# Kernel tuning notes

Hardware: AMD Instinct MI355X
Metric: run time of the kernel (lower is better)

The kernel has to match this reference:

```python
import jax, jax.numpy as jnp
import numpy as np

N, C, H, W = 64, 64, 128, 128
KH, KW = 3, 3


def setup_inputs() -> dict:
    key = jax.random.key(0)
    k1, k2 = jax.random.split(key)
    images = jax.random.normal(k1, (N, C, H, W), dtype=jnp.float32)
    kernels = jax.random.normal(k2, (N, C, KH, KW), dtype=jnp.float32)
    return {"images": images, "kernels": kernels}


def reference(images, kernels):
    # Per-sample conv: image i ([C,H,W]) convolved with kernel i ([C,kh,kw]) -> 1 channel.
    # Equivalent to a grouped conv with N groups:
    #   input  [1, N*C, H, W], weights [N, C, kh, kw], feature_group_count=N
    n, c, h, w = images.shape
    x = images.reshape(1, n * c, h, w)
    out = jax.lax.conv_general_dilated(
        x, kernels,
        window_strides=(1, 1),
        padding='VALID',
        dimension_numbers=('NCHW', 'OIHW', 'NCHW'),
        feature_group_count=n,
    )  # [1, N, H', W']
    return out.reshape(n, 1, out.shape[2], out.shape[3])
```

## Files before the change

kernel.cpp:

```cpp
#include <hip/hip_runtime.h>


#define NS   64
#define CCH  64
#define HH   128
#define WW   128
#define OHH  126
#define OWW  126
#define CHS  (HH * WW)

__global__ __launch_bounds__(512, 4)
void ImageWiseConv2d_direct(const float* __restrict__ img,
                            const float* __restrict__ ker,
                            float* __restrict__ out)
{
    const int tid = threadIdx.x;
    const int bx  = blockIdx.x;
    const int bt  = bx & 7;
    const int n   = bx >> 3;
    const int h0  = bt * 16;

    const int r0 = tid >> 5;
    const int c0 = (tid & 31) << 2;

    int ihr = h0 + r0;
    if (ihr > HH - 3) ihr = HH - 3;
    const int bOff = (c0 < 124) ? 4 : 2;

    const float* p0 = img + (((n * CCH) * HH) + ihr) * WW + c0;
    const float* kp = ker + (n * CCH) * 9;

    float a0 = 0.f, a1 = 0.f, a2 = 0.f, a3 = 0.f;

    float4 A0, A1, A2;
    float2 B0, B1, B2;
    A0 = *(const float4*)(p0);
    A1 = *(const float4*)(p0 + WW);
    A2 = *(const float4*)(p0 + 2 * WW);
    B0 = *(const float2*)(p0 + bOff);
    B1 = *(const float2*)(p0 + WW + bOff);
    B2 = *(const float2*)(p0 + 2 * WW + bOff);

    for (int c = 0; c < CCH; ++c) {
        float4 nA0, nA1, nA2;
        float2 nB0, nB1, nB2;
        const bool more = (c + 1 < CCH);
        if (more) {
            const float* q = p0 + (c + 1) * CHS;
            nA0 = *(const float4*)(q);
            nA1 = *(const float4*)(q + WW);
            nA2 = *(const float4*)(q + 2 * WW);
            nB0 = *(const float2*)(q + bOff);
            nB1 = *(const float2*)(q + WW + bOff);
            nB2 = *(const float2*)(q + 2 * WW + bOff);
        }

        const float w0 = kp[c * 9 + 0], w1 = kp[c * 9 + 1], w2 = kp[c * 9 + 2];
        const float w3 = kp[c * 9 + 3], w4 = kp[c * 9 + 4], w5 = kp[c * 9 + 5];
        const float w6 = kp[c * 9 + 6], w7 = kp[c * 9 + 7], w8 = kp[c * 9 + 8];

        {
            const float v0 = A0.x, v1 = A0.y, v2 = A0.z, v3 = A0.w, v4 = B0.x, v5 = B0.y;
            a0 = fmaf(w0, v0, a0); a0 = fmaf(w1, v1, a0); a0 = fmaf(w2, v2, a0);
            a1 = fmaf(w0, v1, a1); a1 = fmaf(w1, v2, a1); a1 = fmaf(w2, v3, a1);
            a2 = fmaf(w0, v2, a2); a2 = fmaf(w1, v3, a2); a2 = fmaf(w2, v4, a2);
            a3 = fmaf(w0, v3, a3); a3 = fmaf(w1, v4, a3); a3 = fmaf(w2, v5, a3);
        }
        {
            const float v0 = A1.x, v1 = A1.y, v2 = A1.z, v3 = A1.w, v4 = B1.x, v5 = B1.y;
            a0 = fmaf(w3, v0, a0); a0 = fmaf(w4, v1, a0); a0 = fmaf(w5, v2, a0);
            a1 = fmaf(w3, v1, a1); a1 = fmaf(w4, v2, a1); a1 = fmaf(w5, v3, a1);
            a2 = fmaf(w3, v2, a2); a2 = fmaf(w4, v3, a2); a2 = fmaf(w5, v4, a2);
            a3 = fmaf(w3, v3, a3); a3 = fmaf(w4, v4, a3); a3 = fmaf(w5, v5, a3);
        }
        {
            const float v0 = A2.x, v1 = A2.y, v2 = A2.z, v3 = A2.w, v4 = B2.x, v5 = B2.y;
            a0 = fmaf(w6, v0, a0); a0 = fmaf(w7, v1, a0); a0 = fmaf(w8, v2, a0);
            a1 = fmaf(w6, v1, a1); a1 = fmaf(w7, v2, a1); a1 = fmaf(w8, v3, a1);
            a2 = fmaf(w6, v2, a2); a2 = fmaf(w7, v3, a2); a2 = fmaf(w8, v4, a2);
            a3 = fmaf(w6, v3, a3); a3 = fmaf(w7, v4, a3); a3 = fmaf(w8, v5, a3);
        }

        if (more) {
            A0 = nA0; A1 = nA1; A2 = nA2;
            B0 = nB0; B1 = nB1; B2 = nB2;
        }
    }

    const int oh = h0 + r0;
    if (oh < OHH) {
        float* o0 = out + (n * OHH + oh) * OWW + c0;
        *(float2*)o0 = make_float2(a0, a1);
        if (c0 < 124) {
            *(float2*)(o0 + 2) = make_float2(a2, a3);
        }
    }
}

extern "C" void kernel_launch(void* const* d_in, const int* in_sizes, int n_in,
                              void* d_out, int out_size, void* d_ws, size_t ws_size,
                              hipStream_t stream) {
    const float* img = (const float*)d_in[0];
    const float* ker = (const float*)d_in[1];
    float* out = (float*)d_out;

    ImageWiseConv2d_direct<<<dim3(NS * 8), dim3(512), 0, stream>>>(img, ker, out);
}
```

Measured before the change: 392.9 us.

## Compute two output rows per thread and fetch halo via lane shuffles

Each thread now computes a 2x4 output tile instead of 1x4. It loads 4 input rows per channel instead of 3 for each single output row, so the overlapping middle rows are reused from registers across both outputs. The float2 halo loads are replaced by __shfl_down from the neighbouring lane, which removes half the global load instructions. Blocks shrink to 256 threads to keep 16 rows per block. This halves total thread count and raises register pressure, which may reduce latency hiding for the streaming loads.

Result: faster. 354.9 us (median of 2 runs) (-9.7%).

```diff
diff --git a/kernel.cpp b/kernel.cpp
--- a/kernel.cpp
+++ b/kernel.cpp
@@ -9,7 +9,7 @@
 #define OWW  126
 #define CHS  (HH * WW)
 
-__global__ __launch_bounds__(512, 4)
+__global__ __launch_bounds__(256, 2)
 void ImageWiseConv2d_direct(const float* __restrict__ img,
                             const float* __restrict__ ker,
                             float* __restrict__ out)
@@ -20,79 +20,95 @@
     const int n   = bx >> 3;
     const int h0  = bt * 16;
 
-    const int r0 = tid >> 5;
+    const int r0 = (tid >> 5) << 1;
     const int c0 = (tid & 31) << 2;
 
     int ihr = h0 + r0;
-    if (ihr > HH - 3) ihr = HH - 3;
-    const int bOff = (c0 < 124) ? 4 : 2;
+    if (ihr > HH - 4) ihr = HH - 4;
 
     const float* p0 = img + (((n * CCH) * HH) + ihr) * WW + c0;
     const float* kp = ker + (n * CCH) * 9;
 
-    float a0 = 0.f, a1 = 0.f, a2 = 0.f, a3 = 0.f;
+    float a00 = 0.f, a01 = 0.f, a02 = 0.f, a03 = 0.f;
+    float a10 = 0.f, a11 = 0.f, a12 = 0.f, a13 = 0.f;
 
-    float4 A0, A1, A2;
-    float2 B0, B1, B2;
+    float4 A0, A1, A2, A3;
     A0 = *(const float4*)(p0);
     A1 = *(const float4*)(p0 + WW);
     A2 = *(const float4*)(p0 + 2 * WW);
-    B0 = *(const float2*)(p0 + bOff);
-    B1 = *(const float2*)(p0 + WW + bOff);
-    B2 = *(const float2*)(p0 + 2 * WW + bOff);
+    A3 = *(const float4*)(p0 + 3 * WW);
 
     for (int c = 0; c < CCH; ++c) {
-        float4 nA0, nA1, nA2;
-        float2 nB0, nB1, nB2;
+        float4 nA0, nA1, nA2, nA3;
         const bool more = (c + 1 < CCH);
         if (more) {
             const float* q = p0 + (c + 1) * CHS;
             nA0 = *(const float4*)(q);
             nA1 = *(const float4*)(q + WW);
             nA2 = *(const float4*)(q + 2 * WW);
-            nB0 = *(const float2*)(q + bOff);
-            nB1 = *(const float2*)(q + WW + bOff);
-            nB2 = *(const float2*)(q + 2 * WW + bOff);
+            nA3 = *(const float4*)(q + 3 * WW);
         }
 
         const float w0 = kp[c * 9 + 0], w1 = kp[c * 9 + 1], w2 = kp[c * 9 + 2];
         const float w3 = kp[c * 9 + 3], w4 = kp[c * 9 + 4], w5 = kp[c * 9 + 5];
         const float w6 = kp[c * 9 + 6], w7 = kp[c * 9 + 7], w8 = kp[c * 9 + 8];
 
+        const float h40 = __shfl_down(A0.x, 1), h50 = __shfl_down(A0.y, 1);
+        const float h41 = __shfl_down(A1.x, 1), h51 = __shfl_down(A1.y, 1);
+        const float h42 = __shfl_down(A2.x, 1), h52 = __shfl_down(A2.y, 1);
+        const float h43 = __shfl_down(A3.x, 1), h53 = __shfl_down(A3.y, 1);
+
         {
-            const float v0 = A0.x, v1 = A0.y, v2 = A0.z, v3 = A0.w, v4 = B0.x, v5 = B0.y;
-            a0 = fmaf(w0, v0, a0); a0 = fmaf(w1, v1, a0); a0 = fmaf(w2, v2, a0);
-            a1 = fmaf(w0, v1, a1); a1 = fmaf(w1, v2, a1); a1 = fmaf(w2, v3, a1);
-            a2 = fmaf(w0, v2, a2); a2 = fmaf(w1, v3, a2); a2 = fmaf(w2, v4, a2);
-            a3 = fmaf(w0, v3, a3); a3 = fmaf(w1, v4, a3); a3 = fmaf(w2, v5, a3);
+            const float v0 = A0.x, v1 = A0.y, v2 = A0.z, v3 = A0.w, v4 = h40, v5 = h50;
+            a00 = fmaf(w0, v0, a00); a00 = fmaf(w1, v1, a00); a00 = fmaf(w2, v2, a00);
+            a01 = fmaf(w0, v1, a01); a01 = fmaf(w1, v2, a01); a01 = fmaf(w2, v3, a01);
+            a02 = fmaf(w0, v2, a02); a02 = fmaf(w1, v3, a02); a02 = fmaf(w2, v4, a02);
+            a03 = fmaf(w0, v3, a03); a03 = fmaf(w1, v4, a03); a03 = fmaf(w2, v5, a03);
         }
         {
-            const float v0 = A1.x, v1 = A1.y, v2 = A1.z, v3 = A1.w, v4 = B1.x, v5 = B1.y;
-            a0 = fmaf(w3, v0, a0); a0 = fmaf(w4, v1, a0); a0 = fmaf(w5, v2, a0);
-            a1 = fmaf(w3, v1, a1); a1 = fmaf(w4, v2, a1); a1 = fmaf(w5, v3, a1);
-            a2 = fmaf(w3, v2, a2); a2 = fmaf(w4, v3, a2); a2 = fmaf(w5, v4, a2);
-            a3 = fmaf(w3, v3, a3); a3 = fmaf(w4, v4, a3); a3 = fmaf(w5, v5, a3);
+            const float v0 = A1.x, v1 = A1.y, v2 = A1.z, v3 = A1.w, v4 = h41, v5 = h51;
+            a00 = fmaf(w3, v0, a00); a00 = fmaf(w4, v1, a00); a00 = fmaf(w5, v2, a00);
+            a01 = fmaf(w3, v1, a01); a01 = fmaf(w4, v2, a01); a01 = fmaf(w5, v3, a01);
+            a02 = fmaf(w3, v2, a02); a02 = fmaf(w4, v3, a02); a02 = fmaf(w5, v4, a02);
+            a03 = fmaf(w3, v3, a03); a03 = fmaf(w4, v4, a03); a03 = fmaf(w5, v5, a03);
+            a10 = fmaf(w0, v0, a10); a10 = fmaf(w1, v1, a10); a10 = fmaf(w2, v2, a10);
+            a11 = fmaf(w0, v1, a11); a11 = fmaf(w1, v2, a11); a11 = fmaf(w2, v3, a11);
+            a12 = fmaf(w0, v2, a12); a12 = fmaf(w1, v3, a12); a12 = fmaf(w2, v4, a12);
+            a13 = fmaf(w0, v3, a13); a13 = fmaf(w1, v4, a13); a13 = fmaf(w2, v5, a13);
         }
         {
-            const float v0 = A2.x, v1 = A2.y, v2 = A2.z, v3 = A2.w, v4 = B2.x, v5 = B2.y;
-            a0 = fmaf(w6, v0, a0); a0 = fmaf(w7, v1, a0); a0 = fmaf(w8, v2, a0);
-            a1 = fmaf(w6, v1, a1); a1 = fmaf(w7, v2, a1); a1 = fmaf(w8, v3, a1);
-            a2 = fmaf(w6, v2, a2); a2 = fmaf(w7, v3, a2); a2 = fmaf(w8, v4, a2);
-            a3 = fmaf(w6, v3, a3); a3 = fmaf(w7, v4, a3); a3 = fmaf(w8, v5, a3);
+            const float v0 = A2.x, v1 = A2.y, v2 = A2.z, v3 = A2.w, v4 = h42, v5 = h52;
+            a00 = fmaf(w6, v0, a00); a00 = fmaf(w7, v1, a00); a00 = fmaf(w8, v2, a00);
+            a01 = fmaf(w6, v1, a01); a01 = fmaf(w7, v2, a01); a01 = fmaf(w8, v3, a01);
+            a02 = fmaf(w6, v2, a02); a02 = fmaf(w7, v3, a02); a02 = fmaf(w8, v4, a02);
+            a03 = fmaf(w6, v3, a03); a03 = fmaf(w7, v4, a03); a03 = fmaf(w8, v5, a03);
+            a10 = fmaf(w3, v0, a10); a10 = fmaf(w4, v1, a10); a10 = fmaf(w5, v2, a10);
+            a11 = fmaf(w3, v1, a11); a11 = fmaf(w4, v2, a11); a11 = fmaf(w5, v3, a11);
+            a12 = fmaf(w3, v2, a12); a12 = fmaf(w4, v3, a12); a12 = fmaf(w5, v4, a12);
+            a13 = fmaf(w3, v3, a13); a13 = fmaf(w4, v4, a13); a13 = fmaf(w5, v5, a13);
+        }
+        {
+            const float v0 = A3.x, v1 = A3.y, v2 = A3.z, v3 = A3.w, v4 = h43, v5 = h53;
+            a10 = fmaf(w6, v0, a10); a10 = fmaf(w7, v1, a10); a10 = fmaf(w8, v2, a10);
+            a11 = fmaf(w6, v1, a11); a11 = fmaf(w7, v2, a11); a11 = fmaf(w8, v3, a11);
+            a12 = fmaf(w6, v2, a12); a12 = fmaf(w7, v3, a12); a12 = fmaf(w8, v4, a12);
+            a13 = fmaf(w6, v3, a13); a13 = fmaf(w7, v4, a13); a13 = fmaf(w8, v5, a13);
         }
 
         if (more) {
-            A0 = nA0; A1 = nA1; A2 = nA2;
-            B0 = nB0; B1 = nB1; B2 = nB2;
+            A0 = nA0; A1 = nA1; A2 = nA2; A3 = nA3;
         }
     }
 
-    const int oh = h0 + r0;
-    if (oh < OHH) {
-        float* o0 = out + (n * OHH + oh) * OWW + c0;
-        *(float2*)o0 = make_float2(a0, a1);
+    const int oh0 = h0 + r0;
+    if (oh0 < OHH) {
+        float* o0 = out + (n * OHH + oh0) * OWW + c0;
+        float* o1 = o0 + OWW;
+        *(float2*)o0 = make_float2(a00, a01);
+        *(float2*)o1 = make_float2(a10, a11);
         if (c0 < 124) {
-            *(float2*)(o0 + 2) = make_float2(a2, a3);
+            *(float2*)(o0 + 2) = make_float2(a02, a03);
+            *(float2*)(o1 + 2) = make_float2(a12, a13);
         }
     }
 }
@@ -104,5 +120,5 @@
     const float* ker = (const float*)d_in[1];
     float* out = (float*)d_out;
 
-    ImageWiseConv2d_direct<<<dim3(NS * 8), dim3(512), 0, stream>>>(img, ker, out);
+    ImageWiseConv2d_direct<<<dim3(NS * 8), dim3(256), 0, stream>>>(img, ker, out);
 }
```
